# Performance work log

Hardware: AMD Instinct MI355X
Metric: run time of the kernel (lower is better)

Reference implementation:

```python
import jax, jax.numpy as jnp
import numpy as np

BS, QLEN, DIM, H = 2, 2048, 2048, 16
DH = DIM // H


def setup_inputs() -> dict:
    key = jax.random.key(0)
    ks = jax.random.split(key, 10)
    s = 0.02
    return {
        "input": jax.random.normal(ks[0], (BS, QLEN, DIM), jnp.float32),
        "mask": jnp.ones((BS, QLEN), jnp.int32),
        "wq": jax.random.normal(ks[1], (DIM, DIM), jnp.float32) * s,
        "bq": jax.random.normal(ks[2], (DIM,), jnp.float32) * s,
        "wk": jax.random.normal(ks[3], (DIM, DIM), jnp.float32) * s,
        "bk": jax.random.normal(ks[4], (DIM,), jnp.float32) * s,
        "wv": jax.random.normal(ks[5], (DIM, DIM), jnp.float32) * s,
        "bv": jax.random.normal(ks[6], (DIM,), jnp.float32) * s,
        "wo": jax.random.normal(ks[7], (DIM, DIM), jnp.float32) * s,
        "bo": jax.random.normal(ks[8], (DIM,), jnp.float32) * s,
    }


def _shape(x, bs):
    # (bs, len, dim) -> (bs, H, len, DH)
    return x.reshape(bs, -1, H, DH).transpose(0, 2, 1, 3)


def reference(input, mask, wq, bq, wk, bk, wv, bv, wo, bo):
    bs, qlen, dim = input.shape
    # torch Linear: y = x @ W.T + b
    q = _shape(input @ wq.T + bq, bs)  # (bs,H,q,dh)
    k = _shape(input @ wk.T + bk, bs)  # (bs,H,k,dh)
    v = _shape(input @ wv.T + bv, bs)  # (bs,H,k,dh)
    q = q / jnp.sqrt(jnp.asarray(DH, q.dtype))
    scores = jnp.einsum("bhqd,bhkd->bhqk", q, k)
    # mask (bs, klen): positions where mask==0 are masked with -inf
    neg = (mask == 0)[:, None, None, :]  # (bs,1,1,klen)
    scores = jnp.where(neg, -jnp.inf, scores)
    weights = jax.nn.softmax(scores.astype(jnp.float32), axis=-1).astype(scores.dtype)
    # dropout p=0 (eval): identity
    context = jnp.einsum("bhqk,bhkd->bhqd", weights, v)
    context = context.transpose(0, 2, 1, 3).reshape(bs, qlen, dim)
    return context @ wo.T + bo
```

## Files before the change

### kernel.cpp

```cpp
#include <hip/hip_runtime.h>
#include <hip/hip_bf16.h>

#define BS 2
#define QLEN 2048
#define DIM 2048
#define H 16
#define DH 128
#define MTOT (BS*QLEN)

#define BM 256
#define BN 128
#define BK 64
#define NT (DIM/BK)

typedef __hip_bfloat16 bf16;
using f32x4 = __attribute__((ext_vector_type(4))) float;
using s16x8 = __attribute__((ext_vector_type(8))) short;

__device__ inline void gload_lds16(const bf16* g, bf16* l) {
    __builtin_amdgcn_global_load_lds(
        (const __attribute__((address_space(1))) void*)g,
        (__attribute__((address_space(3))) void*)l,
        16, 0, 0);
}

__global__ __launch_bounds__(256) void cast6(
    const float* __restrict__ x,
    const float* __restrict__ w0, const float* __restrict__ w1,
    const float* __restrict__ w2, const float* __restrict__ w3,
    bf16* xo, bf16* o0, bf16* o1, bf16* o2, bf16* o3, int n4)
{
    const float* in; bf16* out;
    switch (blockIdx.y) {
        case 0:  in = w0; out = o0; break;
        case 1:  in = w1; out = o1; break;
        case 2:  in = w2; out = o2; break;
        case 3:  in = w3; out = o3; break;
        case 4:  in = x;        out = xo;        break;
        default: in = x + 4*(size_t)n4; out = xo + 4*(size_t)n4; break;
    }
    int i = blockIdx.x * 256 + threadIdx.x;
    if (i < n4) {
        float4 v = ((const float4*)in)[i];
        __hip_bfloat162 p0 = __float22bfloat162_rn(make_float2(v.x, v.y));
        __hip_bfloat162 p1 = __float22bfloat162_rn(make_float2(v.z, v.w));
        ((__hip_bfloat162*)out)[2*i]   = p0;
        ((__hip_bfloat162*)out)[2*i+1] = p1;
    }
}

__global__ __launch_bounds__(512, 2) void gemm_qkv(
    const bf16* __restrict__ A,
    const bf16* __restrict__ Wq, const bf16* __restrict__ Wk, const bf16* __restrict__ Wv,
    const float* __restrict__ bq, const float* __restrict__ bk, const float* __restrict__ bv,
    bf16* __restrict__ Qo, bf16* __restrict__ Ko, bf16* __restrict__ Vo,
    float qscale)
{
    __shared__ __align__(16) bf16 smem[3*BM*BK + 3*BN*BK];
    bf16* const SA = smem;
    bf16* const SB = smem + 3*BM*BK;

    const int z = blockIdx.z;
    const bf16*  B    = (z == 0) ? Wq : (z == 1) ? Wk : Wv;
    const float* bias = (z == 0) ? bq : (z == 1) ? bk : bv;
    const float  scale = (z == 0) ? qscale : 1.0f;

    const int t = threadIdx.x;
    const int lane = t & 63, w = t >> 6;
    const int row16 = lane & 15, quad = lane >> 4;
    const int sid = blockIdx.y * gridDim.x + blockIdx.x;
    const int swz = (sid & 7) * 32 + (sid >> 3);
    const int m0 = (swz >> 4) * BM, n0 = (swz & 15) * BN;
    const int mo = (w >> 1) * 64, no = (w & 1) * 64;

    auto stageA = [&](int kt, int bufi) {
        bf16* dst = SA + bufi * (BM*BK);
        #pragma unroll
        for (int i = 0; i < 4; i++) {
            int idx = i*512 + t;
            int row = idx >> 3, g = idx & 7;
            int src = g ^ (row & 7);
            gload_lds16(A + (size_t)(m0 + row) * DIM + kt + src*8, dst + idx*8);
        }
    };
    auto stageB = [&](int kt, int bufi) {
        bf16* dst = SB + bufi * (BN*BK);
        #pragma unroll
        for (int i = 0; i < 2; i++) {
            int idx = i*512 + t;
            int row = idx >> 3, g = idx & 7;
            int src = g ^ (row & 7);
            gload_lds16(B + (size_t)(n0 + row) * DIM + kt + src*8, dst + idx*8);
        }
    };

    f32x4 acc[4][4];
    for (int i = 0; i < 4; i++)
        for (int j = 0; j < 4; j++)
            acc[i][j] = (f32x4){0.f, 0.f, 0.f, 0.f};

    stageA(0,    0); stageB(0,    0);
    stageA(BK,   1); stageB(BK,   1);
    stageA(2*BK, 2); stageB(2*BK, 2);
    asm volatile("s_waitcnt vmcnt(12)" ::: "memory");
    __builtin_amdgcn_s_barrier();
    asm volatile("" ::: "memory");

    int buf = 0;
    for (int J = 0; J < NT; ++J) {
        const bf16* Asb = SA + buf * (BM*BK);
        const bf16* Bsb = SB + buf * (BN*BK);

        s16x8 af0[4], bf0[4];
        #pragma unroll
        for (int mt = 0; mt < 4; mt++)
            af0[mt] = *(const s16x8*)&Asb[(mo + mt*16 + row16)*BK + ((quad ^ (row16&7)))*8];
        #pragma unroll
        for (int nt = 0; nt < 4; nt++)
            bf0[nt] = *(const s16x8*)&Bsb[(no + nt*16 + row16)*BK + ((quad ^ (row16&7)))*8];
        if (J >= 1 && J + 2 < NT) {
            int sl = (buf == 0) ? 2 : buf - 1;
            stageA((J+2)*BK, sl); stageB((J+2)*BK, sl);
        }
        asm volatile("" ::: "memory");
        __builtin_amdgcn_s_barrier();
        asm volatile("s_waitcnt lgkmcnt(0)" ::: "memory");
        __builtin_amdgcn_sched_barrier(0);
        __builtin_amdgcn_s_setprio(1);
        #pragma unroll
        for (int mt = 0; mt < 4; mt++)
            #pragma unroll
            for (int nt = 0; nt < 4; nt++)
                acc[mt][nt] = __builtin_amdgcn_mfma_f32_16x16x32_bf16(
                    af0[mt], bf0[nt], acc[mt][nt], 0, 0, 0);
        __builtin_amdgcn_s_setprio(0);
        asm volatile("" ::: "memory");
        __builtin_amdgcn_s_barrier();
        asm volatile("" ::: "memory");

        s16x8 af1[4], bf1[4];
        #pragma unroll
        for (int mt = 0; mt < 4; mt++)
            af1[mt] = *(const s16x8*)&Asb[(mo + mt*16 + row16)*BK + (((4+quad) ^ (row16&7)))*8];
        #pragma unroll
        for (int nt = 0; nt < 4; nt++)
            bf1[nt] = *(const s16x8*)&Bsb[(no + nt*16 + row16)*BK + (((4+quad) ^ (row16&7)))*8];
        asm volatile("" ::: "memory");
        __builtin_amdgcn_s_barrier();
        asm volatile("s_waitcnt lgkmcnt(0)" ::: "memory");
        __builtin_amdgcn_sched_barrier(0);
        __builtin_amdgcn_s_setprio(1);
        #pragma unroll
        for (int mt = 0; mt < 4; mt++)
            #pragma unroll
            for (int nt = 0; nt < 4; nt++)
                acc[mt][nt] = __builtin_amdgcn_mfma_f32_16x16x32_bf16(
                    af1[mt], bf1[nt], acc[mt][nt], 0, 0, 0);
        __builtin_amdgcn_s_setprio(0);
        if (J < NT-2)
            asm volatile("s_waitcnt vmcnt(6)" ::: "memory");
        else if (J == NT-2)
            asm volatile("s_waitcnt vmcnt(0)" ::: "memory");
        if (J < NT-1) {
            asm volatile("" ::: "memory");
            __builtin_amdgcn_s_barrier();
            asm volatile("" ::: "memory");
        }
        buf = (buf == 2) ? 0 : buf + 1;
    }

    if (z < 2) {
        bf16* out = (z == 0) ? Qo : Ko;
        for (int mt = 0; mt < 4; mt++)
            for (int nt = 0; nt < 4; nt++) {
                int n = n0 + no + nt*16 + row16;
                float bv_ = bias[n];
                for (int r = 0; r < 4; r++) {
                    int m = m0 + mo + mt*16 + quad*4 + r;
                    out[(size_t)m * DIM + n] = __float2bfloat16((acc[mt][nt][r] + bv_) * scale);
                }
            }
    } else {
        __syncthreads();
        bf16* Ts = smem;
        for (int mt = 0; mt < 4; mt++)
            for (int nt = 0; nt < 4; nt++) {
                int nn = no + nt*16 + row16;
                float bv_ = bias[n0 + nn];
                for (int r = 0; r < 4; r++) {
                    int mm = mo + mt*16 + quad*4 + r;
                    Ts[nn*264 + mm] = __float2bfloat16(acc[mt][nt][r] + bv_);
                }
            }
        __syncthreads();
        const int b = m0 >> 11, q0b = m0 & 2047;
        #pragma unroll
        for (int i = 0; i < 8; i++) {
            int chunk = i*512 + t;
            int row = chunk >> 5;
            int c = chunk & 31;
            s16x8 val = *(const s16x8*)&Ts[row*264 + c*8];
            *(s16x8*)(Vo + ((size_t)(b*DIM + n0 + row))*QLEN + q0b + c*8) = val;
        }
    }
}

__global__ __launch_bounds__(512, 2) void gemm_out(
    const bf16* __restrict__ A, const bf16* __restrict__ B,
    const float* __restrict__ bias, float* __restrict__ out)
{
    __shared__ __align__(16) bf16 smem[3*BM*BK + 3*BN*BK];
    bf16* const SA = smem;
    bf16* const SB = smem + 3*BM*BK;

    const int t = threadIdx.x;
    const int lane = t & 63, w = t >> 6;
    const int row16 = lane & 15, quad = lane >> 4;
    const int sid = blockIdx.y * gridDim.x + blockIdx.x;
    const int swz = (sid & 7) * 32 + (sid >> 3);
    const int m0 = (swz >> 4) * BM, n0 = (swz & 15) * BN;
    const int mo = (w >> 1) * 64, no = (w & 1) * 64;

    auto stageA = [&](int kt, int bufi) {
        bf16* dst = SA + bufi * (BM*BK);
        #pragma unroll
        for (int i = 0; i < 4; i++) {
            int idx = i*512 + t;
            int row = idx >> 3, g = idx & 7;
            int src = g ^ (row & 7);
            gload_lds16(A + (size_t)(m0 + row) * DIM + kt + src*8, dst + idx*8);
        }
    };
    auto stageB = [&](int kt, int bufi) {
        bf16* dst = SB + bufi * (BN*BK);
        #pragma unroll
        for (int i = 0; i < 2; i++) {
            int idx = i*512 + t;
            int row = idx >> 3, g = idx & 7;
            int src = g ^ (row & 7);
            gload_lds16(B + (size_t)(n0 + row) * DIM + kt + src*8, dst + idx*8);
        }
    };

    f32x4 acc[4][4];
    for (int i = 0; i < 4; i++)
        for (int j = 0; j < 4; j++)
            acc[i][j] = (f32x4){0.f, 0.f, 0.f, 0.f};

    stageA(0,    0); stageB(0,    0);
    stageA(BK,   1); stageB(BK,   1);
    stageA(2*BK, 2); stageB(2*BK, 2);
    asm volatile("s_waitcnt vmcnt(12)" ::: "memory");
    __builtin_amdgcn_s_barrier();
    asm volatile("" ::: "memory");

    int buf = 0;
    for (int J = 0; J < NT; ++J) {
        const bf16* Asb = SA + buf * (BM*BK);
        const bf16* Bsb = SB + buf * (BN*BK);

        s16x8 af0[4], bf0[4];
        #pragma unroll
        for (int mt = 0; mt < 4; mt++)
            af0[mt] = *(const s16x8*)&Asb[(mo + mt*16 + row16)*BK + ((quad ^ (row16&7)))*8];
        #pragma unroll
        for (int nt = 0; nt < 4; nt++)
            bf0[nt] = *(const s16x8*)&Bsb[(no + nt*16 + row16)*BK + ((quad ^ (row16&7)))*8];
        if (J >= 1 && J + 2 < NT) {
            int sl = (buf == 0) ? 2 : buf - 1;
            stageA((J+2)*BK, sl); stageB((J+2)*BK, sl);
        }
        asm volatile("" ::: "memory");
        __builtin_amdgcn_s_barrier();
        asm volatile("s_waitcnt lgkmcnt(0)" ::: "memory");
        __builtin_amdgcn_sched_barrier(0);
        __builtin_amdgcn_s_setprio(1);
        #pragma unroll
        for (int mt = 0; mt < 4; mt++)
            #pragma unroll
            for (int nt = 0; nt < 4; nt++)
                acc[mt][nt] = __builtin_amdgcn_mfma_f32_16x16x32_bf16(
                    af0[mt], bf0[nt], acc[mt][nt], 0, 0, 0);
        __builtin_amdgcn_s_setprio(0);
        asm volatile("" ::: "memory");
        __builtin_amdgcn_s_barrier();
        asm volatile("" ::: "memory");

        s16x8 af1[4], bf1[4];
        #pragma unroll
        for (int mt = 0; mt < 4; mt++)
            af1[mt] = *(const s16x8*)&Asb[(mo + mt*16 + row16)*BK + (((4+quad) ^ (row16&7)))*8];
        #pragma unroll
        for (int nt = 0; nt < 4; nt++)
            bf1[nt] = *(const s16x8*)&Bsb[(no + nt*16 + row16)*BK + (((4+quad) ^ (row16&7)))*8];
        asm volatile("" ::: "memory");
        __builtin_amdgcn_s_barrier();
        asm volatile("s_waitcnt lgkmcnt(0)" ::: "memory");
        __builtin_amdgcn_sched_barrier(0);
        __builtin_amdgcn_s_setprio(1);
        #pragma unroll
        for (int mt = 0; mt < 4; mt++)
            #pragma unroll
            for (int nt = 0; nt < 4; nt++)
                acc[mt][nt] = __builtin_amdgcn_mfma_f32_16x16x32_bf16(
                    af1[mt], bf1[nt], acc[mt][nt], 0, 0, 0);
        __builtin_amdgcn_s_setprio(0);
        if (J < NT-2)
            asm volatile("s_waitcnt vmcnt(6)" ::: "memory");
        else if (J == NT-2)
            asm volatile("s_waitcnt vmcnt(0)" ::: "memory");
        if (J < NT-1) {
            asm volatile("" ::: "memory");
            __builtin_amdgcn_s_barrier();
            asm volatile("" ::: "memory");
        }
        buf = (buf == 2) ? 0 : buf + 1;
    }

    for (int mt = 0; mt < 4; mt++)
        for (int nt = 0; nt < 4; nt++) {
            int n = n0 + no + nt*16 + row16;
            float bv_ = bias[n];
            for (int r = 0; r < 4; r++) {
                int m = m0 + mo + mt*16 + quad*4 + r;
                out[(size_t)m * DIM + n] = acc[mt][nt][r] + bv_;
            }
        }
}

__global__ __launch_bounds__(256, 2) void attn(
    const bf16* __restrict__ Q, const bf16* __restrict__ Kb,
    const bf16* __restrict__ Vt, const int* __restrict__ mask,
    bf16* __restrict__ Ctx)
{
    __shared__ __align__(16) bf16 Ks[2][64*128];
    __shared__ __align__(16) bf16 Vs[128*64];
    __shared__ __align__(16) bf16 Pl[4][32*64];

    const int t = threadIdx.x, w = t >> 6, lane = t & 63;
    const int row16 = lane & 15, quad = lane >> 4;
    const int sid = blockIdx.y * gridDim.x + blockIdx.x;
    const int swz = (sid & 7) * 64 + (sid >> 3);
    const int bh = swz >> 4, b = bh >> 4, h = bh & 15;
    const int q0 = (swz & 15) * 128 + w * 32;

    s16x8 qf[2][4];
    for (int qs = 0; qs < 2; qs++) {
        const bf16* qp = Q + (size_t)(b*QLEN + q0 + qs*16 + row16) * DIM + h*DH;
        for (int ks = 0; ks < 4; ks++)
            qf[qs][ks] = *(const s16x8*)(qp + ks*32 + quad*8);
    }

    f32x4 o[2][8];
    for (int qs = 0; qs < 2; qs++)
        for (int i = 0; i < 8; i++) o[qs][i] = (f32x4){0.f, 0.f, 0.f, 0.f};
    float lsum[2][4] = {{0.f,0.f,0.f,0.f},{0.f,0.f,0.f,0.f}};
    const int* mrow = mask + b * QLEN;

    const bf16* Kbase = Kb + (size_t)b*QLEN*DIM + h*DH;
    const bf16* Vbase = Vt + ((size_t)b*DIM + h*DH) * QLEN;

    #pragma unroll
    for (int i = 0; i < 4; i++) {
        int idx = i*256 + t;
        int kr = idx >> 4, kc = idx & 15;
        int kg = kc ^ (kr & 15);
        gload_lds16(Kbase + (size_t)kr * DIM + kg*8, &Ks[0][idx*8]);
    }

    for (int it = 0; it < QLEN/64; it++) {
        const int kt = it * 64, buf = it & 1;
        __syncthreads();

        if (it + 1 < QLEN/64) {
            #pragma unroll
            for (int i = 0; i < 4; i++) {
                int idx = i*256 + t;
                int kr = idx >> 4, kc = idx & 15;
                int kg = kc ^ (kr & 15);
                gload_lds16(Kbase + (size_t)(kt + 64 + kr) * DIM + kg*8, &Ks[buf^1][idx*8]);
            }
        }
        #pragma unroll
        for (int i = 0; i < 4; i++) {
            int idx = i*256 + t;
            int vd = idx >> 3, vc = idx & 7;
            int vg = vc ^ (vd & 7);
            gload_lds16(Vbase + (size_t)vd * QLEN + kt + vg*8, &Vs[idx*8]);
        }

        float mval[4];
        #pragma unroll
        for (int nt = 0; nt < 4; nt++)
            mval[nt] = (mrow[kt + nt*16 + row16] != 0) ? -20.0f : -1e30f;

        f32x4 sc[2][4];
        for (int qs = 0; qs < 2; qs++)
            for (int nt = 0; nt < 4; nt++) sc[qs][nt] = (f32x4){0.f, 0.f, 0.f, 0.f};
        #pragma unroll
        for (int ks = 0; ks < 4; ks++) {
            #pragma unroll
            for (int nt = 0; nt < 4; nt++) {
                int rrow = nt*16 + row16;
                int c = (ks*4 + quad) ^ row16;
                s16x8 kf = *(const s16x8*)&Ks[buf][rrow*128 + c*8];
                sc[0][nt] = __builtin_amdgcn_mfma_f32_16x16x32_bf16(qf[0][ks], kf, sc[0][nt], 0, 0, 0);
                sc[1][nt] = __builtin_amdgcn_mfma_f32_16x16x32_bf16(qf[1][ks], kf, sc[1][nt], 0, 0, 0);
            }
        }

        #pragma unroll
        for (int qs = 0; qs < 2; qs++) {
            #pragma unroll
            for (int r = 0; r < 4; r++) {
                int prow = qs*16 + quad*4 + r;
                float ts = 0.f;
                #pragma unroll
                for (int nt = 0; nt < 4; nt++) {
                    float p = exp2f(sc[qs][nt][r] + mval[nt]);
                    ts += p;
                    int chunk = nt*2 + (row16 >> 3);
                    int slot = chunk ^ (prow & 7);
                    Pl[w][prow*64 + slot*8 + (row16 & 7)] = __float2bfloat16(p);
                }
                lsum[qs][r] += ts;
            }
        }

        __syncthreads();

        #pragma unroll
        for (int kc = 0; kc < 2; kc++) {
            int pslot0 = ((kc*4 + quad) ^ (row16 & 7));
            s16x8 pf0 = *(const s16x8*)&Pl[w][(0*16 + row16)*64 + pslot0*8];
            s16x8 pf1 = *(const s16x8*)&Pl[w][(1*16 + row16)*64 + pslot0*8];
            #pragma unroll
            for (int nt = 0; nt < 8; nt++) {
                int d = nt*16 + row16;
                int c = (kc*4 + quad) ^ (d & 7);
                s16x8 vf = *(const s16x8*)&Vs[d*64 + c*8];
                o[0][nt] = __builtin_amdgcn_mfma_f32_16x16x32_bf16(pf0, vf, o[0][nt], 0, 0, 0);
                o[1][nt] = __builtin_amdgcn_mfma_f32_16x16x32_bf16(pf1, vf, o[1][nt], 0, 0, 0);
            }
        }
    }

    for (int qs = 0; qs < 2; qs++) {
        float inv[4];
        for (int r = 0; r < 4; r++) {
            float ts = lsum[qs][r];
            ts += __shfl_xor(ts, 1);
            ts += __shfl_xor(ts, 2);
            ts += __shfl_xor(ts, 4);
            ts += __shfl_xor(ts, 8);
            inv[r] = 1.0f / ts;
        }
        for (int nt = 0; nt < 8; nt++)
            for (int r = 0; r < 4; r++) {
                float v = o[qs][nt][r] * inv[r];
                Ctx[(size_t)(b*QLEN + q0 + qs*16 + quad*4 + r) * DIM + h*DH + nt*16 + row16] =
                    __float2bfloat16(v);
            }
    }
}

extern "C" void kernel_launch(void* const* d_in, const int* in_sizes, int n_in,
                              void* d_out, int out_size, void* d_ws, size_t ws_size,
                              hipStream_t stream) {
    const float* x    = (const float*)d_in[0];
    const int*   mask = (const int*)d_in[1];
    const float* wq   = (const float*)d_in[2];
    const float* bq   = (const float*)d_in[3];
    const float* wk   = (const float*)d_in[4];
    const float* bk   = (const float*)d_in[5];
    const float* wv   = (const float*)d_in[6];
    const float* bv   = (const float*)d_in[7];
    const float* wo   = (const float*)d_in[8];
    const float* bo   = (const float*)d_in[9];

    char* ws = (char*)d_ws;
    const size_t MB = 1024 * 1024;
    bf16* Xb  = (bf16*)(ws);
    bf16* Qb  = (bf16*)(ws + 16*MB);
    bf16* Kb  = (bf16*)(ws + 32*MB);
    bf16* Vtb = (bf16*)(ws + 48*MB);
    bf16* Wqb = (bf16*)(ws + 64*MB);
    bf16* Wkb = (bf16*)(ws + 72*MB);
    bf16* Wvb = (bf16*)(ws + 80*MB);
    bf16* Wob = (bf16*)(ws + 88*MB);
    bf16* Ctx = Xb;

    int n4w = (DIM*DIM) / 4;
    cast6<<<dim3(n4w/256, 6), 256, 0, stream>>>(x, wq, wk, wv, wo,
                                                Xb, Wqb, Wkb, Wvb, Wob, n4w);

    const float qscale = 0.08838834764831845f * 1.4426950408889634f;
    gemm_qkv<<<dim3(DIM/BN, MTOT/BM, 3), 512, 0, stream>>>(
        Xb, Wqb, Wkb, Wvb, bq, bk, bv, Qb, Kb, Vtb, qscale);

    attn<<<dim3(QLEN/128, BS*H), 256, 0, stream>>>(Qb, Kb, Vtb, mask, Ctx);

    gemm_out<<<dim3(DIM/BN, MTOT/BM), 512, 0, stream>>>(Ctx, Wob, bo, (float*)d_out);
}
```

Baseline: 396.9 us.

## Split QKV GEMM into 256x256-tile Q/K kernel and separate V kernel

The fused QKV projection is split in two. Q and K now come from a new kernel with 256x256 tiles, double-buffered LDS, and staging interleaved across four sub-phases of MFMA work. V keeps the old 256x128 transposed-store path in its own launch. Larger tiles raise arithmetic intensity and cut global traffic for Q/K, at the cost of an extra launch, more accumulator registers, and fewer blocks (256 for Q/K), which may leave the 256 CUs underfilled.

```diff
diff --git a/kernel.cpp b/kernel.cpp
--- a/kernel.cpp
+++ b/kernel.cpp
@@ -49,21 +49,149 @@
     }
 }
 
-__global__ __launch_bounds__(512, 2) void gemm_qkv(
+__global__ __launch_bounds__(512, 2) void gemm_qk(
     const bf16* __restrict__ A,
-    const bf16* __restrict__ Wq, const bf16* __restrict__ Wk, const bf16* __restrict__ Wv,
-    const float* __restrict__ bq, const float* __restrict__ bk, const float* __restrict__ bv,
-    bf16* __restrict__ Qo, bf16* __restrict__ Ko, bf16* __restrict__ Vo,
+    const bf16* __restrict__ Wq, const bf16* __restrict__ Wk,
+    const float* __restrict__ bq, const float* __restrict__ bk,
+    bf16* __restrict__ Qo, bf16* __restrict__ Ko,
     float qscale)
+{
+    __shared__ __align__(16) bf16 smem[2*256*64*2];
+    bf16* const SA = smem;
+    bf16* const SB = smem + 2*256*64;
+
+    const int t = threadIdx.x;
+    const int lane = t & 63, w = t >> 6;
+    const int row16 = lane & 15, quad = lane >> 4;
+
+    const int sid = (blockIdx.z * 16 + blockIdx.y) * 8 + blockIdx.x;
+    const int swz = (sid & 7) * 32 + (sid >> 3);
+    const int zz = swz >> 7;
+    const int m0 = ((swz >> 3) & 15) * 256;
+    const int n0 = (swz & 7) * 256;
+    const int mo = (w >> 2) * 128, no = (w & 3) * 64;
+
+    const bf16*  Bw   = (zz == 0) ? Wq : Wk;
+    const float* bias = (zz == 0) ? bq : bk;
+    const float  scale = (zz == 0) ? qscale : 1.0f;
+
+    auto stageA_part = [&](int kt, int bufi, int h) {
+        bf16* dst = SA + bufi * (256*64);
+        #pragma unroll
+        for (int i = 0; i < 2; i++) {
+            int c = i*512 + t;
+            int rp = c >> 3, g = c & 7;
+            int row = (rp & 63) + ((rp & 64) << 1) + h*64;
+            int src = g ^ (row & 7);
+            gload_lds16(A + (size_t)(m0 + row) * DIM + kt + src*8, dst + (row*8 + g)*8);
+        }
+    };
+    auto stageB_half = [&](int kt, int bufi, int h) {
+        bf16* dst = SB + bufi * (256*64);
+        #pragma unroll
+        for (int i = 0; i < 2; i++) {
+            int c = i*512 + t;
+            int rp = c >> 3, g = c & 7;
+            int row = rp + h*128;
+            int src = g ^ (row & 7);
+            gload_lds16(Bw + (size_t)(n0 + row) * DIM + kt + src*8, dst + (row*8 + g)*8);
+        }
+    };
+
+    f32x4 acc[8][4];
+    #pragma unroll
+    for (int i = 0; i < 8; i++)
+        #pragma unroll
+        for (int j = 0; j < 4; j++)
+            acc[i][j] = (f32x4){0.f, 0.f, 0.f, 0.f};
+
+    stageB_half(0, 0, 0); stageB_half(0, 0, 1);
+    stageA_part(0, 0, 0); stageA_part(0, 0, 1);
+    asm volatile("s_waitcnt vmcnt(0)" ::: "memory");
+    __builtin_amdgcn_s_barrier();
+    asm volatile("" ::: "memory");
+
+    for (int J = 0; J < NT; ++J) {
+        const bf16* Asb = SA + (J & 1) * (256*64);
+        const bf16* Bsb = SB + (J & 1) * (256*64);
+        const int stbuf = (J + 1) & 1;
+        const bool st = (J + 1 < NT);
+        s16x8 bfr[4][2];
+
+        #pragma unroll
+        for (int p = 0; p < 4; ++p) {
+            s16x8 af[2][2];
+            #pragma unroll
+            for (int i = 0; i < 2; i++)
+                #pragma unroll
+                for (int kk = 0; kk < 2; kk++)
+                    af[i][kk] = *(const s16x8*)&Asb[(mo + (2*p+i)*16 + row16)*64 +
+                                                    (((kk*4+quad) ^ (row16&7)))*8];
+            if (p == 0) {
+                #pragma unroll
+                for (int nj = 0; nj < 4; nj++)
+                    #pragma unroll
+                    for (int kk = 0; kk < 2; kk++)
+                        bfr[nj][kk] = *(const s16x8*)&Bsb[(no + nj*16 + row16)*64 +
+                                                          (((kk*4+quad) ^ (row16&7)))*8];
+            }
+            if (st) {
+                if      (p == 0) stageB_half((J+1)*BK, stbuf, 0);
+                else if (p == 1) stageB_half((J+1)*BK, stbuf, 1);
+                else if (p == 2) stageA_part((J+1)*BK, stbuf, 0);
+                else             stageA_part((J+1)*BK, stbuf, 1);
+            }
+            if (p == 1) {
+                if (J < NT-1) asm volatile("s_waitcnt vmcnt(4)" ::: "memory");
+                else          asm volatile("s_waitcnt vmcnt(0)" ::: "memory");
+            }
+            if (p == 3 && J < NT-1)
+                asm volatile("s_waitcnt vmcnt(2)" ::: "memory");
+
+            asm volatile("" ::: "memory");
+            __builtin_amdgcn_s_barrier();
+            asm volatile("s_waitcnt lgkmcnt(0)" ::: "memory");
+            __builtin_amdgcn_sched_barrier(0);
+            __builtin_amdgcn_s_setprio(1);
+            #pragma unroll
+            for (int kk = 0; kk < 2; kk++)
+                #pragma unroll
+                for (int i = 0; i < 2; i++)
+                    #pragma unroll
+                    for (int nj = 0; nj < 4; nj++)
+                        acc[2*p+i][nj] = __builtin_amdgcn_mfma_f32_16x16x32_bf16(
+                            af[i][kk], bfr[nj][kk], acc[2*p+i][nj], 0, 0, 0);
+            __builtin_amdgcn_s_setprio(0);
+            if (!(p == 3 && J == NT-1)) {
+                asm volatile("" ::: "memory");
+                __builtin_amdgcn_s_barrier();
+                asm volatile("" ::: "memory");
+            }
+        }
+    }
+
+    bf16* out = (zz == 0) ? Qo : Ko;
+    #pragma unroll
+    for (int mi = 0; mi < 8; mi++)
+        #pragma unroll
+        for (int nj = 0; nj < 4; nj++) {
+            int n = n0 + no + nj*16 + row16;
+            float bv_ = bias[n];
+            #pragma unroll
+            for (int r = 0; r < 4; r++) {
+                int m = m0 + mo + mi*16 + quad*4 + r;
+                out[(size_t)m * DIM + n] = __float2bfloat16((acc[mi][nj][r] + bv_) * scale);
+            }
+        }
+}
+
+__global__ __launch_bounds__(512, 2) void gemm_v(
+    const bf16* __restrict__ A, const bf16* __restrict__ B,
+    const float* __restrict__ bias, bf16* __restrict__ Vo)
 {
     __shared__ __align__(16) bf16 smem[3*BM*BK + 3*BN*BK];
     bf16* const SA = smem;
     bf16* const SB = smem + 3*BM*BK;
-
-    const int z = blockIdx.z;
-    const bf16*  B    = (z == 0) ? Wq : (z == 1) ? Wk : Wv;
-    const float* bias = (z == 0) ? bq : (z == 1) ? bk : bv;
-    const float  scale = (z == 0) ? qscale : 1.0f;
 
     const int t = threadIdx.x;
     const int lane = t & 63, w = t >> 6;
@@ -169,39 +297,26 @@
         buf = (buf == 2) ? 0 : buf + 1;
     }
 
-    if (z < 2) {
-        bf16* out = (z == 0) ? Qo : Ko;
-        for (int mt = 0; mt < 4; mt++)
-            for (int nt = 0; nt < 4; nt++) {
-                int n = n0 + no + nt*16 + row16;
-                float bv_ = bias[n];
-                for (int r = 0; r < 4; r++) {
-                    int m = m0 + mo + mt*16 + quad*4 + r;
-                    out[(size_t)m * DIM + n] = __float2bfloat16((acc[mt][nt][r] + bv_) * scale);
-                }
-            }
-    } else {
-        __syncthreads();
-        bf16* Ts = smem;
-        for (int mt = 0; mt < 4; mt++)
-            for (int nt = 0; nt < 4; nt++) {
-                int nn = no + nt*16 + row16;
-                float bv_ = bias[n0 + nn];
-                for (int r = 0; r < 4; r++) {
-                    int mm = mo + mt*16 + quad*4 + r;
-                    Ts[nn*264 + mm] = __float2bfloat16(acc[mt][nt][r] + bv_);
-                }
-            }
-        __syncthreads();
-        const int b = m0 >> 11, q0b = m0 & 2047;
-        #pragma unroll
-        for (int i = 0; i < 8; i++) {
-            int chunk = i*512 + t;
-            int row = chunk >> 5;
-            int c = chunk & 31;
-            s16x8 val = *(const s16x8*)&Ts[row*264 + c*8];
-            *(s16x8*)(Vo + ((size_t)(b*DIM + n0 + row))*QLEN + q0b + c*8) = val;
-        }
+    __syncthreads();
+    bf16* Ts = smem;
+    for (int mt = 0; mt < 4; mt++)
+        for (int nt = 0; nt < 4; nt++) {
+            int nn = no + nt*16 + row16;
+            float bv_ = bias[n0 + nn];
+            for (int r = 0; r < 4; r++) {
+                int mm = mo + mt*16 + quad*4 + r;
+                Ts[nn*264 + mm] = __float2bfloat16(acc[mt][nt][r] + bv_);
+            }
+        }
+    __syncthreads();
+    const int b = m0 >> 11, q0b = m0 & 2047;
+    #pragma unroll
+    for (int i = 0; i < 8; i++) {
+        int chunk = i*512 + t;
+        int row = chunk >> 5;
+        int c = chunk & 31;
+        s16x8 val = *(const s16x8*)&Ts[row*264 + c*8];
+        *(s16x8*)(Vo + ((size_t)(b*DIM + n0 + row))*QLEN + q0b + c*8) = val;
     }
 }
 
@@ -495,8 +610,10 @@
                                                 Xb, Wqb, Wkb, Wvb, Wob, n4w);
 
     const float qscale = 0.08838834764831845f * 1.4426950408889634f;
-    gemm_qkv<<<dim3(DIM/BN, MTOT/BM, 3), 512, 0, stream>>>(
-        Xb, Wqb, Wkb, Wvb, bq, bk, bv, Qb, Kb, Vtb, qscale);
+    gemm_qk<<<dim3(8, 16, 2), 512, 0, stream>>>(
+        Xb, Wqb, Wkb, bq, bk, Qb, Kb, qscale);
+
+    gemm_v<<<dim3(DIM/BN, MTOT/BM), 512, 0, stream>>>(Xb, Wvb, bv, Vtb);
 
     attn<<<dim3(QLEN/128, BS*H), 256, 0, stream>>>(Qb, Kb, Vtb, mask, Ctx);
 
```

Result: no change. 394.7 us (-0.5%).
